# Kernel tuning notes

Measured on AMD Instinct MI355X. Metric: run time of the kernel, lower is better.

## Reference

```python
import jax, jax.numpy as jnp
import numpy as np

T, D, H, KEXP = 91, 256, 4, 4
DH = D // H
NA, NRG = 128, 1024
NEG = -1e10
SCALE = 2.0  # sqrt(head_num=4), faithful to the original (NOT sqrt(dh))


def _ln(x, g, b, eps=1e-5):
    m = jnp.mean(x, axis=-1, keepdims=True)
    v = jnp.mean((x - m) ** 2, axis=-1, keepdims=True)
    return (x - m) * jax.lax.rsqrt(v + eps) * g + b


def setup_inputs() -> dict:
    key = jax.random.key(0)
    ks = jax.random.split(key, 16)
    s = lambda fan_in: 1.0 / np.sqrt(fan_in)
    inp = {
        "agent": jax.random.normal(ks[0], (NA, T, D), jnp.float32),
        "rg": jax.random.normal(ks[1], (NRG, T, D), jnp.float32),
        "ln_x_g": jnp.ones((D,), jnp.float32),
        "ln_x_b": jnp.zeros((D,), jnp.float32),
        "wk": jax.random.uniform(ks[2], (D, D), jnp.float32, -s(D), s(D)),
        "bk": jnp.zeros((D,), jnp.float32),
        "wv": jax.random.uniform(ks[3], (D, D), jnp.float32, -s(D), s(D)),
        "bv": jnp.zeros((D,), jnp.float32),
        "wq": jax.random.uniform(ks[4], (D, D), jnp.float32, -s(D), s(D)),
        "bq": jnp.zeros((D,), jnp.float32),
        "q_scale": jnp.full((DH,), 0.001, jnp.float32),
        "wy": jax.random.uniform(ks[5], (D, D), jnp.float32, -s(D), s(D)),
        "by": jnp.zeros((D,), jnp.float32),
        "wf1": jax.random.uniform(ks[6], (D, KEXP * D), jnp.float32, -s(D), s(D)),
        "bf1": jnp.zeros((KEXP * D,), jnp.float32),
        "wf2": jax.random.uniform(ks[7], (KEXP * D, D), jnp.float32, -s(KEXP * D), s(KEXP * D)),
        "bf2": jnp.zeros((D,), jnp.float32),
        "ln_z_g": jnp.ones((D,), jnp.float32),
        "ln_z_b": jnp.zeros((D,), jnp.float32),
        "agent_rg_mask": jax.random.randint(ks[8], (T, NA, NRG), 0, 2).astype(bool),
        "padding_mask": jax.random.randint(ks[9], (T, NRG), 0, 2).astype(bool),
        "rg_valid_mask": jax.random.randint(ks[10], (T, NA), 0, 2).astype(bool),
    }
    return inp


def reference(agent, rg, ln_x_g, ln_x_b, wk, bk, wv, bv, wq, bq, q_scale,
              wy, by, wf1, bf1, wf2, bf2, ln_z_g, ln_z_b,
              agent_rg_mask, padding_mask, rg_valid_mask):
    agent_n = _ln(agent, ln_x_g, ln_x_b)   # (Na, T, D)
    rg_n = _ln(rg, ln_x_g, ln_x_b)         # (Nrg, T, D)

    K = jax.nn.relu(rg_n @ wk + bk).reshape(NRG, T, H, DH)
    V = jax.nn.relu(rg_n @ wv + bv).reshape(NRG, T, H, DH)
    Q = jax.nn.relu(agent_n @ wq + bq).reshape(NA, T, H, DH) * q_scale

    # energy: (T, H, Na, Nrg)
    energy = jnp.einsum("athd,rthd->thar", Q, K) / SCALE
    energy = jnp.where(agent_rg_mask[:, None, :, :], energy, NEG)
    energy = jnp.where(padding_mask[:, None, None, :], energy, NEG)
    energy = jnp.where(rg_valid_mask[:, None, :, None], energy, NEG)
    attn = jax.nn.softmax(energy, axis=-1)

    Y1 = jnp.einsum("thar,rthd->athd", attn, V).reshape(NA, T, D)
    Y2 = jax.nn.relu(Y1 @ wy + by)
    S = Y2 + agent_n
    F1 = jax.nn.relu(S @ wf1 + bf1)
    F2 = jax.nn.relu(F1 @ wf2 + bf2)
    Z = _ln(F2, ln_z_g, ln_z_b)

    Qp = jnp.transpose(Q, (1, 2, 0, 3))  # (T,H,Na,dh)
    Kp = jnp.transpose(K, (1, 2, 0, 3))
    Vp = jnp.transpose(V, (1, 2, 0, 3))
    return (Z, Qp, Kp, Vp)
```

## Files before the change

kernel.cpp:

```cpp
#include <hip/hip_runtime.h>

#define T_   91
#define D_   256
#define H_   4
#define DH_  64
#define NA_  128
#define NRG_ 1024
#define KEXP_ 4

typedef float f32x4 __attribute__((ext_vector_type(4)));
typedef short bf16x8 __attribute__((ext_vector_type(8)));

static constexpr float P_EPS = 1.3877787807814457e-17f;

__device__ inline ushort f2bf(float f) {
    union { float f; unsigned u; } v; v.f = f;
    unsigned r = (v.u + 0x7fffu + ((v.u >> 16) & 1u)) >> 16;
    return (ushort)r;
}
__device__ inline unsigned pk2(float a, float b) {
    return (unsigned)f2bf(a) | ((unsigned)f2bf(b) << 16);
}
__device__ inline float bf2f(ushort b) {
    union { unsigned u; float f; } v; v.u = ((unsigned)b) << 16;
    return v.f;
}

__global__ __launch_bounds__(256) void ln_norm(
    const float* __restrict__ agent, const float* __restrict__ rg,
    const float* __restrict__ g, const float* __restrict__ b,
    ushort* __restrict__ agn, ushort* __restrict__ rgn) {
    int row = blockIdx.x * 4 + (threadIdx.x >> 6);
    int lane = threadIdx.x & 63;
    bool is_a = row < NA_ * T_;
    const float* src = is_a ? (agent + (size_t)row * D_)
                            : (rg + (size_t)(row - NA_ * T_) * D_);
    f32x4 x = *(const f32x4*)(src + lane * 4);
    float s1 = x[0] + x[1] + x[2] + x[3];
    float s2 = x[0] * x[0] + x[1] * x[1] + x[2] * x[2] + x[3] * x[3];
#pragma unroll
    for (int off = 1; off < 64; off <<= 1) {
        s1 += __shfl_xor(s1, off);
        s2 += __shfl_xor(s2, off);
    }
    float mean = s1 * (1.0f / 256.0f);
    float var = s2 * (1.0f / 256.0f) - mean * mean;
    float rstd = rsqrtf(var + 1e-5f);
    f32x4 gv = *(const f32x4*)(g + lane * 4);
    f32x4 bv = *(const f32x4*)(b + lane * 4);
    float y0 = (x[0] - mean) * rstd * gv[0] + bv[0];
    float y1 = (x[1] - mean) * rstd * gv[1] + bv[1];
    float y2 = (x[2] - mean) * rstd * gv[2] + bv[2];
    float y3 = (x[3] - mean) * rstd * gv[3] + bv[3];
    ushort* dst = is_a ? (agn + (size_t)row * D_)
                       : (rgn + (size_t)(row - NA_ * T_) * D_);
    *(uint2*)(dst + lane * 4) = make_uint2(pk2(y0, y1), pk2(y2, y3));
}

__global__ void prep_w(const float* __restrict__ W, ushort* __restrict__ dst,
                       int K, int N) {
    int idx = blockIdx.x * 256 + threadIdx.x;
    int n = idx / K, k = idx % K;
    dst[idx] = f2bf(W[(size_t)k * N + n]);
}

__global__ __launch_bounds__(256) void pack_mask(
    const int* __restrict__ am, const int* __restrict__ pm,
    const int* __restrict__ vmk, unsigned* __restrict__ cm) {
    int base = blockIdx.x * 4;
    int t = base / NA_;
    int w = threadIdx.x >> 6, lane = threadIdx.x & 63;
    __shared__ int pmS[NRG_];
#pragma unroll
    for (int i = 0; i < 4; ++i)
        pmS[threadIdx.x + i * 256] = pm[(size_t)t * NRG_ + threadIdx.x + i * 256];
    __syncthreads();
    int idx = base + w;
    int a = idx & (NA_ - 1);
    int valid = vmk[t * NA_ + a];
    const int* amrow = am + (size_t)idx * NRG_;
#pragma unroll
    for (int c = 0; c < 16; ++c) {
        int r = c * 64 + lane;
        bool bit = valid && amrow[r] && pmS[r];
        unsigned long long msk = __ballot(bit);
        if (lane == 0) {
            cm[(size_t)idx * 32 + c * 2]     = (unsigned)msk;
            cm[(size_t)idx * 32 + c * 2 + 1] = (unsigned)(msk >> 32);
        }
    }
}

__global__ __launch_bounds__(512) void gemm_wide(
    const ushort* __restrict__ Ab, const ushort* __restrict__ Bt,
    const float* __restrict__ bias0, const float* __restrict__ bias1,
    const float* __restrict__ aux0, const ushort* __restrict__ residb,
    float* __restrict__ out0, float* __restrict__ out1,
    ushort* __restrict__ out2, ushort* __restrict__ out3,
    int N, int K, int mode) {
    __shared__ ushort smem[64 * 72 + 256 * 72];
    __shared__ float lnp[2][64][4];
    ushort (*As)[72] = (ushort(*)[72])smem;
    ushort (*Bs)[72] = (ushort(*)[72])(smem + 64 * 72);
    float (*Et)[68] = (float(*)[68])smem;

    int bxi = blockIdx.x, by = blockIdx.y;
    int bn = bxi * 256;
    int bm = by * 64;
    int t = 0, rb = 0, a0 = 0;
    if (mode == 1) { t = by >> 4; rb = (by & 15) << 6; }
    else if (mode == 2) { t = by >> 1; a0 = (by & 1) << 6; }

    int tid = threadIdx.x;
    int w = tid >> 6, lane = tid & 63;
    int wm = w >> 2, wn = w & 3;
    int l15 = lane & 15, l4 = lane >> 4;

    f32x4 acc[2][4];
#pragma unroll
    for (int i = 0; i < 2; ++i)
#pragma unroll
        for (int j = 0; j < 4; ++j)
#pragma unroll
            for (int r = 0; r < 4; ++r) acc[i][j][r] = 0.0f;

    for (int k0 = 0; k0 < K; k0 += 64) {
        {
            int row = tid >> 3, c8 = (tid & 7) * 8;
            size_t arow = (mode == 1) ? ((size_t)(rb + row) * T_ + t)
                        : (mode == 2) ? ((size_t)(a0 + row) * T_ + t)
                        : (size_t)(bm + row);
            *(bf16x8*)&As[row][c8] = *(const bf16x8*)(Ab + arow * K + k0 + c8);
        }
#pragma unroll
        for (int it = 0; it < 4; ++it) {
            int li = tid + it * 512;
            int row = li >> 3, c8 = (li & 7) * 8;
            *(bf16x8*)&Bs[row][c8] =
                *(const bf16x8*)(Bt + (size_t)(bn + row) * K + k0 + c8);
        }
        __syncthreads();
#pragma unroll
        for (int kk = 0; kk < 2; ++kk) {
            bf16x8 af[2], bfr[4];
#pragma unroll
            for (int i = 0; i < 2; ++i)
                af[i] = *(const bf16x8*)&As[wm * 32 + i * 16 + l15][kk * 32 + l4 * 8];
#pragma unroll
            for (int j = 0; j < 4; ++j)
                bfr[j] = *(const bf16x8*)&Bs[wn * 64 + j * 16 + l15][kk * 32 + l4 * 8];
#pragma unroll
            for (int i = 0; i < 2; ++i)
#pragma unroll
                for (int j = 0; j < 4; ++j)
                    acc[i][j] = __builtin_amdgcn_mfma_f32_16x16x32_bf16(
                        af[i], bfr[j], acc[i][j], 0, 0, 0);
        }
        __syncthreads();
    }

    float v[2][4][4];
#pragma unroll
    for (int i = 0; i < 2; ++i)
#pragma unroll
        for (int j = 0; j < 4; ++j)
#pragma unroll
            for (int reg = 0; reg < 4; ++reg) {
                int nl = wn * 64 + j * 16 + l15;
                int rowl = wm * 32 + i * 16 + l4 * 4 + reg;
                float bs;
                if (mode == 1) bs = bxi ? bias1[nl] : bias0[nl];
                else if (mode == 0) bs = bias0[bn + nl];
                else bs = bias0[nl];
                float x = fmaxf(acc[i][j][reg] + bs, 0.0f);
                if (mode == 2) x *= aux0[nl & 63];
                if (mode == 3) x += bf2f(residb[(size_t)(bm + rowl) * 256 + nl]);
                v[i][j][reg] = x;
            }

    if (mode == 5) {
        float rs_[2][4], rq_[2][4];
#pragma unroll
        for (int i = 0; i < 2; ++i)
#pragma unroll
            for (int reg = 0; reg < 4; ++reg) {
                float s = 0.0f, q = 0.0f;
#pragma unroll
                for (int j = 0; j < 4; ++j) {
                    float x = v[i][j][reg];
                    s += x; q += x * x;
                }
#pragma unroll
                for (int off = 1; off < 16; off <<= 1) {
                    s += __shfl_xor(s, off);
                    q += __shfl_xor(q, off);
                }
                rs_[i][reg] = s; rq_[i][reg] = q;
            }
        if (l15 == 0) {
#pragma unroll
            for (int i = 0; i < 2; ++i)
#pragma unroll
                for (int reg = 0; reg < 4; ++reg) {
                    int row = wm * 32 + i * 16 + l4 * 4 + reg;
                    lnp[0][row][wn] = rs_[i][reg];
                    lnp[1][row][wn] = rq_[i][reg];
                }
        }
        __syncthreads();
#pragma unroll
        for (int i = 0; i < 2; ++i)
#pragma unroll
            for (int reg = 0; reg < 4; ++reg) {
                int row = wm * 32 + i * 16 + l4 * 4 + reg;
                float S1 = lnp[0][row][0] + lnp[0][row][1] + lnp[0][row][2] + lnp[0][row][3];
                float S2 = lnp[1][row][0] + lnp[1][row][1] + lnp[1][row][2] + lnp[1][row][3];
                float mean = S1 * (1.0f / 256.0f);
                float var = S2 * (1.0f / 256.0f) - mean * mean;
                float rstd = rsqrtf(var + 1e-5f);
#pragma unroll
                for (int j = 0; j < 4; ++j) {
                    int nl = wn * 64 + j * 16 + l15;
                    float z = (v[i][j][reg] - mean) * rstd * bias1[nl] + aux0[nl];
                    out0[(size_t)(bm + row) * 256 + nl] = z;
                }
            }
        return;
    }

#pragma unroll 1
    for (int jq = 0; jq < 4; ++jq) {
        __syncthreads();
        if (wn == jq) {
#pragma unroll
            for (int i = 0; i < 2; ++i)
#pragma unroll
                for (int j = 0; j < 4; ++j)
#pragma unroll
                    for (int reg = 0; reg < 4; ++reg)
                        Et[wm * 32 + i * 16 + l4 * 4 + reg][j * 16 + l15] = v[i][j][reg];
        }
        __syncthreads();

        if (mode == 1) {
            size_t base = (((size_t)t * H_ + jq) * NRG_ + rb) * DH_;
            float* of = bxi ? out1 : out0;
#pragma unroll
            for (int it = 0; it < 2; ++it) {
                int slot = it * 512 + tid;
                int row = slot >> 4, c4 = (slot & 15) * 4;
                *(f32x4*)(of + base + row * 64 + c4) = *(f32x4*)&Et[row][c4];
            }
            if (!bxi) {
#pragma unroll
                for (int it = 0; it < 2; ++it) {
                    int slot = it * 512 + tid;
                    int row = slot >> 4, c4 = (slot & 15) * 4;
                    uint2 u = make_uint2(pk2(Et[row][c4], Et[row][c4 + 1]),
                                         pk2(Et[row][c4 + 2], Et[row][c4 + 3]));
                    *(uint2*)(out2 + base + row * 64 + c4) = u;
                }
            } else {
                __syncthreads();
                if (wn == jq) {
#pragma unroll
                    for (int i = 0; i < 2; ++i)
#pragma unroll
                        for (int j = 0; j < 4; ++j)
#pragma unroll
                            for (int reg = 0; reg < 4; ++reg)
                                Et[j * 16 + l15][wm * 32 + i * 16 + l4 * 4 + reg] = v[i][j][reg];
                }
                __syncthreads();
                size_t tb = ((size_t)t * H_ + jq) * DH_ * NRG_;
#pragma unroll
                for (int it = 0; it < 2; ++it) {
                    int slot = it * 512 + tid;
                    int d = slot >> 4, r4 = (slot & 15) * 4;
                    uint2 u = make_uint2(pk2(Et[d][r4], Et[d][r4 + 1]),
                                         pk2(Et[d][r4 + 2], Et[d][r4 + 3]));
                    *(uint2*)(out3 + tb + (size_t)d * NRG_ + rb + r4) = u;
                }
            }
        } else if (mode == 2) {
            size_t base = (((size_t)t * H_ + jq) * NA_ + a0) * DH_;
#pragma unroll
            for (int it = 0; it < 2; ++it) {
                int slot = it * 512 + tid;
                int row = slot >> 4, c4 = (slot & 15) * 4;
                *(f32x4*)(out0 + base + row * 64 + c4) = *(f32x4*)&Et[row][c4];
                uint2 u = make_uint2(pk2(Et[row][c4] * 0.5f, Et[row][c4 + 1] * 0.5f),
                                     pk2(Et[row][c4 + 2] * 0.5f, Et[row][c4 + 3] * 0.5f));
                *(uint2*)(out2 + base + row * 64 + c4) = u;
            }
        } else {
#pragma unroll
            for (int it = 0; it < 2; ++it) {
                int slot = it * 512 + tid;
                int row = slot >> 4, c4 = (slot & 15) * 4;
                uint2 u = make_uint2(pk2(Et[row][c4], Et[row][c4 + 1]),
                                     pk2(Et[row][c4 + 2], Et[row][c4 + 3]));
                *(uint2*)(out2 + (size_t)(bm + row) * N + bn + jq * 64 + c4) = u;
            }
        }
    }
}

__global__ __launch_bounds__(256) void attn_flash(
    const ushort* __restrict__ Qb, const ushort* __restrict__ Kb,
    const ushort* __restrict__ Vtb, const unsigned* __restrict__ cm,
    ushort* __restrict__ Y1b) {
    int ah = blockIdx.x;
    int th = blockIdx.y;
    int t = th >> 2, h = th & 3;
    int tid = threadIdx.x;
    int w = tid >> 6, lane = tid & 63;
    int l15 = lane & 15, l4 = lane >> 4;

    __shared__ ushort Ks[64][72];
    __shared__ ushort Vts[64][72];
    __shared__ ushort Ps[64][72];
    __shared__ unsigned cmw[64][2];

    bf16x8 qf[2];
#pragma unroll
    for (int kk = 0; kk < 2; ++kk)
        qf[kk] = *(const bf16x8*)(Qb + ((size_t)th * NA_ + ah * 64 + w * 16 + l15) * DH_
                                  + kk * 32 + l4 * 8);

    f32x4 o[4];
    float rsum[4] = {0.0f, 0.0f, 0.0f, 0.0f};
#pragma unroll
    for (int ds = 0; ds < 4; ++ds)
#pragma unroll
        for (int r = 0; r < 4; ++r) o[ds][r] = 0.0f;

    for (int rt = 0; rt < 16; ++rt) {
        int r0 = rt * 64;
#pragma unroll
        for (int it = 0; it < 2; ++it) {
            int li = tid + it * 256;
            int row = li >> 3, c8 = (li & 7) * 8;
            *(bf16x8*)&Ks[row][c8] =
                *(const bf16x8*)(Kb + ((size_t)th * NRG_ + r0 + row) * DH_ + c8);
            *(bf16x8*)&Vts[row][c8] =
                *(const bf16x8*)(Vtb + ((size_t)th * DH_ + row) * NRG_ + r0 + c8);
        }
        if (tid < 128) {
            int a = tid >> 1, wd = tid & 1;
            cmw[a][wd] = cm[((size_t)t * NA_ + ah * 64 + a) * 32 + rt * 2 + wd];
        }
        __syncthreads();

        f32x4 e[4];
#pragma unroll
        for (int rs = 0; rs < 4; ++rs) {
#pragma unroll
            for (int r = 0; r < 4; ++r) e[rs][r] = 0.0f;
#pragma unroll
            for (int kk = 0; kk < 2; ++kk) {
                bf16x8 kf = *(const bf16x8*)&Ks[rs * 16 + l15][kk * 32 + l4 * 8];
                e[rs] = __builtin_amdgcn_mfma_f32_16x16x32_bf16(qf[kk], kf, e[rs], 0, 0, 0);
            }
        }

#pragma unroll
        for (int reg = 0; reg < 4; ++reg) {
            int a_loc = w * 16 + l4 * 4 + reg;
            unsigned w0 = cmw[a_loc][0], w1 = cmw[a_loc][1];
#pragma unroll
            for (int rs = 0; rs < 4; ++rs) {
                unsigned wd = (rs & 2) ? w1 : w0;
                int bit = (wd >> ((rs & 1) * 16 + l15)) & 1;
                float p = bit ? __expf(e[rs][reg]) : P_EPS;
                rsum[reg] += p;
                Ps[a_loc][rs * 16 + l15] = f2bf(p);
            }
        }

#pragma unroll
        for (int rc = 0; rc < 2; ++rc) {
            bf16x8 pa = *(const bf16x8*)&Ps[w * 16 + l15][rc * 32 + l4 * 8];
#pragma unroll
            for (int ds = 0; ds < 4; ++ds) {
                bf16x8 vf = *(const bf16x8*)&Vts[ds * 16 + l15][rc * 32 + l4 * 8];
                o[ds] = __builtin_amdgcn_mfma_f32_16x16x32_bf16(pa, vf, o[ds], 0, 0, 0);
            }
        }
        __syncthreads();
    }

#pragma unroll
    for (int off = 1; off < 16; off <<= 1)
#pragma unroll
        for (int reg = 0; reg < 4; ++reg)
            rsum[reg] += __shfl_xor(rsum[reg], off);
    float rinv[4];
#pragma unroll
    for (int reg = 0; reg < 4; ++reg) rinv[reg] = 1.0f / rsum[reg];

#pragma unroll
    for (int ds = 0; ds < 4; ++ds)
#pragma unroll
        for (int reg = 0; reg < 4; ++reg) {
            int a_g = ah * 64 + w * 16 + l4 * 4 + reg;
            int d = ds * 16 + l15;
            Y1b[((size_t)a_g * T_ + t) * D_ + h * DH_ + d] = f2bf(o[ds][reg] * rinv[reg]);
        }
}

extern "C" void kernel_launch(void* const* d_in, const int* in_sizes, int n_in,
                              void* d_out, int out_size, void* d_ws, size_t ws_size,
                              hipStream_t stream) {
    const float* agent   = (const float*)d_in[0];
    const float* rg      = (const float*)d_in[1];
    const float* ln_x_g  = (const float*)d_in[2];
    const float* ln_x_b  = (const float*)d_in[3];
    const float* wk      = (const float*)d_in[4];
    const float* bk      = (const float*)d_in[5];
    const float* wv      = (const float*)d_in[6];
    const float* bv      = (const float*)d_in[7];
    const float* wq      = (const float*)d_in[8];
    const float* bq      = (const float*)d_in[9];
    const float* q_scale = (const float*)d_in[10];
    const float* wy      = (const float*)d_in[11];
    const float* by      = (const float*)d_in[12];
    const float* wf1     = (const float*)d_in[13];
    const float* bf1     = (const float*)d_in[14];
    const float* wf2     = (const float*)d_in[15];
    const float* bf2     = (const float*)d_in[16];
    const float* ln_z_g  = (const float*)d_in[17];
    const float* ln_z_b  = (const float*)d_in[18];
    const int*   am      = (const int*)d_in[19];
    const int*   pm      = (const int*)d_in[20];
    const int*   vmk     = (const int*)d_in[21];

    float* Z  = (float*)d_out;
    float* Qp = Z + (size_t)NA_ * T_ * D_;
    float* Kp = Qp + (size_t)NA_ * T_ * D_;
    float* Vp = Kp + (size_t)NRG_ * T_ * D_;

    char* p = (char*)d_ws;
    ushort* rgn_b = (ushort*)p;   p += (size_t)NRG_ * T_ * D_ * 2;
    ushort* agn_b = (ushort*)p;   p += (size_t)NA_ * T_ * D_ * 2;
    ushort* wkvt  = (ushort*)p;   p += (size_t)512 * 256 * 2;
    ushort* wqt   = (ushort*)p;   p += (size_t)256 * 256 * 2;
    ushort* wyt   = (ushort*)p;   p += (size_t)256 * 256 * 2;
    ushort* wf1t  = (ushort*)p;   p += (size_t)1024 * 256 * 2;
    ushort* wf2t  = (ushort*)p;   p += (size_t)256 * 1024 * 2;
    unsigned* cm  = (unsigned*)p; p += (size_t)T_ * NA_ * 32 * 4;
    ushort* Kb    = (ushort*)p;   p += (size_t)T_ * H_ * NRG_ * DH_ * 2;
    ushort* Vtb   = (ushort*)p;   p += (size_t)T_ * H_ * NRG_ * DH_ * 2;
    ushort* Qb    = (ushort*)p;   p += (size_t)T_ * H_ * NA_ * DH_ * 2;
    ushort* Y1b   = (ushort*)p;   p += (size_t)NA_ * T_ * D_ * 2;
    ushort* Sb    = (ushort*)p;   p += (size_t)NA_ * T_ * D_ * 2;

    ushort* F1b = rgn_b;

    dim3 blk(256), wblk(512);

    ln_norm<<<dim3((NA_ + NRG_) * T_ / 4), blk, 0, stream>>>(
        agent, rg, ln_x_g, ln_x_b, agn_b, rgn_b);

    prep_w<<<dim3(256), blk, 0, stream>>>(wk, wkvt, 256, 256);
    prep_w<<<dim3(256), blk, 0, stream>>>(wv, wkvt + 65536, 256, 256);
    prep_w<<<dim3(256), blk, 0, stream>>>(wq, wqt, 256, 256);
    prep_w<<<dim3(256), blk, 0, stream>>>(wy, wyt, 256, 256);
    prep_w<<<dim3(1024), blk, 0, stream>>>(wf1, wf1t, 256, 1024);
    prep_w<<<dim3(1024), blk, 0, stream>>>(wf2, wf2t, 1024, 256);

    pack_mask<<<dim3(T_ * NA_ / 4), blk, 0, stream>>>(am, pm, vmk, cm);

    gemm_wide<<<dim3(2, T_ * 16), wblk, 0, stream>>>(
        rgn_b, wkvt, bk, bv, nullptr, nullptr,
        Kp, Vp, Kb, Vtb, 512, 256, 1);

    gemm_wide<<<dim3(1, T_ * 2), wblk, 0, stream>>>(
        agn_b, wqt, bq, nullptr, q_scale, nullptr,
        Qp, nullptr, Qb, nullptr, 256, 256, 2);

    attn_flash<<<dim3(2, T_ * H_), blk, 0, stream>>>(Qb, Kb, Vtb, cm, Y1b);

    gemm_wide<<<dim3(1, NA_ * T_ / 64), wblk, 0, stream>>>(
        Y1b, wyt, by, nullptr, nullptr, agn_b,
        nullptr, nullptr, Sb, nullptr, 256, 256, 3);

    gemm_wide<<<dim3(4, NA_ * T_ / 64), wblk, 0, stream>>>(
        Sb, wf1t, bf1, nullptr, nullptr, nullptr,
        nullptr, nullptr, F1b, nullptr, 1024, 256, 0);

    gemm_wide<<<dim3(1, NA_ * T_ / 64), wblk, 0, stream>>>(
        F1b, wf2t, bf2, ln_z_g, ln_z_b, nullptr,
        Z, nullptr, nullptr, nullptr, 256, 1024, 5);
}
```

Baseline: 302.1 us.

## Merge weight prep launches, swizzle KV GEMM grid, widen attention blocks to all agents

Replaces six weight-transpose launches with one combined kernel to cut launch overhead. The K/V projection GEMM now uses a 1D grid whose block order groups eight row tiles per N-half, aiming for better L2 reuse of the A tiles. The attention kernel now processes all 128 agents per (t,h) block with 512 threads, so K/V tiles are loaded once instead of twice, at the cost of half as many blocks and more shared memory per block.

```diff
diff --git a/kernel.cpp b/kernel.cpp
--- a/kernel.cpp
+++ b/kernel.cpp
@@ -57,11 +57,36 @@
     *(uint2*)(dst + lane * 4) = make_uint2(pk2(y0, y1), pk2(y2, y3));
 }
 
-__global__ void prep_w(const float* __restrict__ W, ushort* __restrict__ dst,
-                       int K, int N) {
+__global__ __launch_bounds__(256) void prep_w_all(
+    const float* __restrict__ wk, const float* __restrict__ wv,
+    const float* __restrict__ wq, const float* __restrict__ wy,
+    const float* __restrict__ wf1, const float* __restrict__ wf2,
+    ushort* __restrict__ wkvt, ushort* __restrict__ wqt,
+    ushort* __restrict__ wyt, ushort* __restrict__ wf1t,
+    ushort* __restrict__ wf2t) {
     int idx = blockIdx.x * 256 + threadIdx.x;
-    int n = idx / K, k = idx % K;
-    dst[idx] = f2bf(W[(size_t)k * N + n]);
+    if (idx < 131072) {
+        const float* W = (idx < 65536) ? wk : wv;
+        int li = idx & 65535;
+        int n = li >> 8, k = li & 255;
+        wkvt[idx] = f2bf(W[(size_t)k * 256 + n]);
+    } else if (idx < 196608) {
+        int li = idx - 131072;
+        int n = li >> 8, k = li & 255;
+        wqt[li] = f2bf(wq[(size_t)k * 256 + n]);
+    } else if (idx < 262144) {
+        int li = idx - 196608;
+        int n = li >> 8, k = li & 255;
+        wyt[li] = f2bf(wy[(size_t)k * 256 + n]);
+    } else if (idx < 524288) {
+        int li = idx - 262144;
+        int n = li >> 8, k = li & 255;
+        wf1t[li] = f2bf(wf1[(size_t)k * 1024 + n]);
+    } else {
+        int li = idx - 524288;
+        int n = li >> 10, k = li & 1023;
+        wf2t[li] = f2bf(wf2[(size_t)k * 256 + n]);
+    }
 }
 
 __global__ __launch_bounds__(256) void pack_mask(
@@ -104,7 +129,15 @@
     ushort (*Bs)[72] = (ushort(*)[72])(smem + 64 * 72);
     float (*Et)[68] = (float(*)[68])smem;
 
-    int bxi = blockIdx.x, by = blockIdx.y;
+    int bxi, by;
+    if (mode == 1) {
+        int wg = blockIdx.x;
+        int sub = wg & 15, pid = wg >> 4;
+        bxi = sub >> 3;
+        by = pid * 8 + (sub & 7);
+    } else {
+        bxi = blockIdx.x; by = blockIdx.y;
+    }
     int bn = bxi * 256;
     int bm = by * 64;
     int t = 0, rb = 0, a0 = 0;
@@ -306,12 +339,11 @@
     }
 }
 
-__global__ __launch_bounds__(256) void attn_flash(
+__global__ __launch_bounds__(512) void attn_flash(
     const ushort* __restrict__ Qb, const ushort* __restrict__ Kb,
     const ushort* __restrict__ Vtb, const unsigned* __restrict__ cm,
     ushort* __restrict__ Y1b) {
-    int ah = blockIdx.x;
-    int th = blockIdx.y;
+    int th = blockIdx.x;
     int t = th >> 2, h = th & 3;
     int tid = threadIdx.x;
     int w = tid >> 6, lane = tid & 63;
@@ -319,13 +351,13 @@
 
     __shared__ ushort Ks[64][72];
     __shared__ ushort Vts[64][72];
-    __shared__ ushort Ps[64][72];
-    __shared__ unsigned cmw[64][2];
+    __shared__ ushort Ps[128][72];
+    __shared__ unsigned cmw[128][2];
 
     bf16x8 qf[2];
 #pragma unroll
     for (int kk = 0; kk < 2; ++kk)
-        qf[kk] = *(const bf16x8*)(Qb + ((size_t)th * NA_ + ah * 64 + w * 16 + l15) * DH_
+        qf[kk] = *(const bf16x8*)(Qb + ((size_t)th * NA_ + w * 16 + l15) * DH_
                                   + kk * 32 + l4 * 8);
 
     f32x4 o[4];
@@ -337,18 +369,16 @@
 
     for (int rt = 0; rt < 16; ++rt) {
         int r0 = rt * 64;
-#pragma unroll
-        for (int it = 0; it < 2; ++it) {
-            int li = tid + it * 256;
-            int row = li >> 3, c8 = (li & 7) * 8;
+        {
+            int row = tid >> 3, c8 = (tid & 7) * 8;
             *(bf16x8*)&Ks[row][c8] =
                 *(const bf16x8*)(Kb + ((size_t)th * NRG_ + r0 + row) * DH_ + c8);
             *(bf16x8*)&Vts[row][c8] =
                 *(const bf16x8*)(Vtb + ((size_t)th * DH_ + row) * NRG_ + r0 + c8);
         }
-        if (tid < 128) {
+        if (tid < 256) {
             int a = tid >> 1, wd = tid & 1;
-            cmw[a][wd] = cm[((size_t)t * NA_ + ah * 64 + a) * 32 + rt * 2 + wd];
+            cmw[a][wd] = cm[((size_t)t * NA_ + a) * 32 + rt * 2 + wd];
         }
         __syncthreads();
 
@@ -403,7 +433,7 @@
     for (int ds = 0; ds < 4; ++ds)
 #pragma unroll
         for (int reg = 0; reg < 4; ++reg) {
-            int a_g = ah * 64 + w * 16 + l4 * 4 + reg;
+            int a_g = w * 16 + l4 * 4 + reg;
             int d = ds * 16 + l15;
             Y1b[((size_t)a_g * T_ + t) * D_ + h * DH_ + d] = f2bf(o[ds][reg] * rinv[reg]);
         }
@@ -462,16 +492,12 @@
     ln_norm<<<dim3((NA_ + NRG_) * T_ / 4), blk, 0, stream>>>(
         agent, rg, ln_x_g, ln_x_b, agn_b, rgn_b);
 
-    prep_w<<<dim3(256), blk, 0, stream>>>(wk, wkvt, 256, 256);
-    prep_w<<<dim3(256), blk, 0, stream>>>(wv, wkvt + 65536, 256, 256);
-    prep_w<<<dim3(256), blk, 0, stream>>>(wq, wqt, 256, 256);
-    prep_w<<<dim3(256), blk, 0, stream>>>(wy, wyt, 256, 256);
-    prep_w<<<dim3(1024), blk, 0, stream>>>(wf1, wf1t, 256, 1024);
-    prep_w<<<dim3(1024), blk, 0, stream>>>(wf2, wf2t, 1024, 256);
+    prep_w_all<<<dim3(3072), blk, 0, stream>>>(
+        wk, wv, wq, wy, wf1, wf2, wkvt, wqt, wyt, wf1t, wf2t);
 
     pack_mask<<<dim3(T_ * NA_ / 4), blk, 0, stream>>>(am, pm, vmk, cm);
 
-    gemm_wide<<<dim3(2, T_ * 16), wblk, 0, stream>>>(
+    gemm_wide<<<dim3(T_ * 32), wblk, 0, stream>>>(
         rgn_b, wkvt, bk, bv, nullptr, nullptr,
         Kp, Vp, Kb, Vtb, 512, 256, 1);
 
@@ -479,7 +505,7 @@
         agn_b, wqt, bq, nullptr, q_scale, nullptr,
         Qp, nullptr, Qb, nullptr, 256, 256, 2);
 
-    attn_flash<<<dim3(2, T_ * H_), blk, 0, stream>>>(Qb, Kb, Vtb, cm, Y1b);
+    attn_flash<<<dim3(T_ * H_), wblk, 0, stream>>>(Qb, Kb, Vtb, cm, Y1b);
 
     gemm_wide<<<dim3(1, NA_ * T_ / 64), wblk, 0, stream>>>(
         Y1b, wyt, by, nullptr, nullptr, agn_b,
```

Result: faster. 292.0 us (-3.4%).
